# Optimization experiments

Hardware: AMD Instinct MI355X
Metric: run time of the kernel (lower is better)

The kernel has to match this reference:

```python
import jax, jax.numpy as jnp
import numpy as np

D_MODEL = 512
N_HEADS = 8
HEAD_DIM = D_MODEL // N_HEADS


def setup_inputs() -> dict:
    key = jax.random.key(0)
    ks = jax.random.split(key, 7)
    x = jax.random.normal(ks[0], (8, 2048, D_MODEL), dtype=jnp.float32)
    ln_gamma = jnp.ones((D_MODEL,), jnp.float32)
    ln_beta = jnp.zeros((D_MODEL,), jnp.float32)
    s = 1.0 / np.sqrt(D_MODEL)
    W_qkv = jax.random.uniform(ks[1], (3 * D_MODEL, D_MODEL), jnp.float32, -s, s)
    b_qkv = jax.random.uniform(ks[2], (3 * D_MODEL,), jnp.float32, -s, s)
    W_out = jax.random.uniform(ks[3], (D_MODEL, D_MODEL), jnp.float32, -s, s)
    b_out = jax.random.uniform(ks[4], (D_MODEL,), jnp.float32, -s, s)
    return {"x": x, "ln_gamma": ln_gamma, "ln_beta": ln_beta,
            "W_qkv": W_qkv, "b_qkv": b_qkv, "W_out": W_out, "b_out": b_out}


def reference(x, ln_gamma, ln_beta, W_qkv, b_qkv, W_out, b_out):
    b, s, d = x.shape
    # LayerNorm (eps=1e-5, torch default)
    mu = jnp.mean(x, axis=-1, keepdims=True)
    var = jnp.mean(jnp.square(x - mu), axis=-1, keepdims=True)
    xn = (x - mu) * jax.lax.rsqrt(var + 1e-5) * ln_gamma + ln_beta
    # QKV projection (torch Linear: x @ W.T + b)
    qkv = xn @ W_qkv.T + b_qkv                       # [b, s, 3d]
    qkv = qkv.reshape(b, s, 3, N_HEADS, HEAD_DIM)
    qkv = jnp.transpose(qkv, (2, 0, 3, 1, 4))        # [3, b, h, s, hd]
    q, k, v = qkv[0], qkv[1], qkv[2]
    scale = HEAD_DIM ** -0.5
    attn = jnp.einsum('bhqd,bhkd->bhqk', q, k) * scale
    attn = jax.nn.softmax(attn, axis=-1)
    out = jnp.einsum('bhqk,bhkd->bhqd', attn, v)     # [b, h, s, hd]
    out = jnp.transpose(out, (0, 2, 1, 3)).reshape(b, s, d)
    return out @ W_out.T + b_out
```

## Files before the change

kernel.cpp:

```cpp
#include <hip/hip_runtime.h>
#include <stdint.h>

#define NH 8
#define HD 64
#define BATCH 8
#define SEQ 2048
#define DM 512
#define TOK (BATCH * SEQ)

#define QSCALE 0.18033688011112042f

typedef __attribute__((ext_vector_type(8))) __bf16 bf16x8;
typedef __attribute__((ext_vector_type(4))) float f32x4;
typedef __attribute__((ext_vector_type(16))) float f32x16;
typedef __attribute__((ext_vector_type(8))) uint16_t u16x8;

__device__ __forceinline__ uint16_t f2bf(float f) {
  union { __bf16 h; uint16_t u; } c;
  c.h = (__bf16)f;
  return c.u;
}

__device__ __forceinline__ void load_lds16(const void* g, void* l) {
  __builtin_amdgcn_global_load_lds(
      (const __attribute__((address_space(1))) void*)g,
      (__attribute__((address_space(3))) void*)l, 16, 0, 0);
}

#define VM_DRAIN() asm volatile("s_waitcnt vmcnt(0)" ::: "memory")

__device__ __forceinline__ int swz128(int row, int kbyte) {
  return (row * 128 + kbyte) ^ ((row & 7) << 4);
}

#define MFMA16(a, b, c) __builtin_amdgcn_mfma_f32_16x16x32_bf16(a, b, c, 0, 0, 0)
#define MFMA32(a, b, c) __builtin_amdgcn_mfma_f32_32x32x16_bf16(a, b, c, 0, 0, 0)

__global__ __launch_bounds__(256) void ln_kernel(
    const float* __restrict__ x, const float* __restrict__ gam,
    const float* __restrict__ bet, uint16_t* __restrict__ xn) {
  const int row = blockIdx.x * 4 + (threadIdx.x >> 6);
  const int lane = threadIdx.x & 63;
  const float4* xr = (const float4*)(x + (size_t)row * DM);
  float4 a0 = xr[lane * 2 + 0];
  float4 a1 = xr[lane * 2 + 1];
  float s = a0.x + a0.y + a0.z + a0.w + a1.x + a1.y + a1.z + a1.w;
  float q = a0.x * a0.x + a0.y * a0.y + a0.z * a0.z + a0.w * a0.w +
            a1.x * a1.x + a1.y * a1.y + a1.z * a1.z + a1.w * a1.w;
#pragma unroll
  for (int m = 1; m < 64; m <<= 1) {
    s += __shfl_xor(s, m);
    q += __shfl_xor(q, m);
  }
  const float mean = s * (1.0f / DM);
  const float var = q * (1.0f / DM) - mean * mean;
  const float rstd = rsqrtf(var + 1e-5f);
  const float4* gv = (const float4*)gam;
  const float4* bv = (const float4*)bet;
  float4 g0 = gv[lane * 2], g1 = gv[lane * 2 + 1];
  float4 b0 = bv[lane * 2], b1 = bv[lane * 2 + 1];
  u16x8 r;
  r[0] = f2bf((a0.x - mean) * rstd * g0.x + b0.x);
  r[1] = f2bf((a0.y - mean) * rstd * g0.y + b0.y);
  r[2] = f2bf((a0.z - mean) * rstd * g0.z + b0.z);
  r[3] = f2bf((a0.w - mean) * rstd * g0.w + b0.w);
  r[4] = f2bf((a1.x - mean) * rstd * g1.x + b1.x);
  r[5] = f2bf((a1.y - mean) * rstd * g1.y + b1.y);
  r[6] = f2bf((a1.z - mean) * rstd * g1.z + b1.z);
  r[7] = f2bf((a1.w - mean) * rstd * g1.w + b1.w);
  *(u16x8*)(xn + (size_t)row * DM + lane * 8) = r;
}

__global__ __launch_bounds__(256) void cast_w(const float* __restrict__ w,
                                              uint16_t* __restrict__ o, int n8) {
  int i = blockIdx.x * 256 + threadIdx.x;
  if (i >= n8) return;
  const float4* p = (const float4*)w + (size_t)i * 2;
  float4 a0 = p[0], a1 = p[1];
  u16x8 r;
  r[0] = f2bf(a0.x); r[1] = f2bf(a0.y); r[2] = f2bf(a0.z); r[3] = f2bf(a0.w);
  r[4] = f2bf(a1.x); r[5] = f2bf(a1.y); r[6] = f2bf(a1.z); r[7] = f2bf(a1.w);
  *(u16x8*)(o + (size_t)i * 8) = r;
}

template <int EPI>
__global__ __launch_bounds__(256) void gemm_nt(
    const uint16_t* __restrict__ A, const uint16_t* __restrict__ Bw,
    const float* __restrict__ bias, uint16_t* __restrict__ oq,
    uint16_t* __restrict__ okk, uint16_t* __restrict__ ov,
    float* __restrict__ oc) {
  __shared__ __align__(16) char As[128 * 64 * 2];
  __shared__ __align__(16) char Bs[128 * 64 * 2];
  const int tid = threadIdx.x;
  const int lane = tid & 63;
  const int w = tid >> 6;
  const int wr = (w >> 1) * 64;
  const int wc = (w & 1) * 64;
  const int l15 = lane & 15;
  const int l4 = lane >> 4;
  const size_t tileM = (size_t)blockIdx.y * 128;
  const int tileN = blockIdx.x * 128;
  const int trow = tid >> 3;
  const int tcol = tid & 7;
  const f32x4 vzero = {0.f, 0.f, 0.f, 0.f};

  f32x4 acc[4][4];
#pragma unroll
  for (int m = 0; m < 4; ++m)
#pragma unroll
    for (int n = 0; n < 4; ++n) acc[m][n] = vzero;

  for (int kt = 0; kt < 8; ++kt) {
    if (kt) __syncthreads();
#pragma unroll
    for (int i = 0; i < 4; ++i) {
      const int row = i * 32 + trow;
      const int c0 = 8 * (tcol ^ (row & 7));
      load_lds16(A + (tileM + row) * DM + kt * 64 + c0, As + i * 4096 + w * 1024);
      load_lds16(Bw + (size_t)(tileN + row) * DM + kt * 64 + c0, Bs + i * 4096 + w * 1024);
    }
    VM_DRAIN();
    __syncthreads();
#pragma unroll
    for (int ks = 0; ks < 2; ++ks) {
      const int kb = ks * 64 + l4 * 16;
      bf16x8 af[4], bfr[4];
#pragma unroll
      for (int m = 0; m < 4; ++m) {
        const int r = wr + m * 16 + l15;
        af[m] = *(const bf16x8*)(As + swz128(r, kb));
      }
#pragma unroll
      for (int n = 0; n < 4; ++n) {
        const int r = wc + n * 16 + l15;
        bfr[n] = *(const bf16x8*)(Bs + swz128(r, kb));
      }
#pragma unroll
      for (int m = 0; m < 4; ++m)
#pragma unroll
        for (int n = 0; n < 4; ++n)
          acc[m][n] = MFMA16(af[m], bfr[n], acc[m][n]);
    }
  }

#pragma unroll
  for (int m = 0; m < 4; ++m) {
    const size_t row0 = tileM + wr + m * 16 + l4 * 4;
#pragma unroll
    for (int n = 0; n < 4; ++n) {
      const int col = tileN + wc + n * 16 + l15;
      const float bb = bias[col];
#pragma unroll
      for (int jj = 0; jj < 4; ++jj) {
        const float val = acc[m][n][jj] + bb;
        const size_t r = row0 + jj;
        if (EPI == 0) {
          const int wh = col >> 9;
          const int rem = col & 511;
          const int h = rem >> 6;
          const int dd = rem & 63;
          const int bi = (int)(r >> 11);
          const int si = (int)(r & 2047);
          const size_t bh = (size_t)bi * NH + h;
          if (wh == 0)
            oq[(bh * SEQ + si) * HD + dd] = f2bf(val * QSCALE);
          else if (wh == 1)
            okk[(bh * SEQ + si) * HD + dd] = f2bf(val);
          else
            ov[(bh * HD + dd) * SEQ + si] = f2bf(val);
        } else {
          oc[r * DM + col] = val;
        }
      }
    }
  }
}

__global__ __launch_bounds__(256) void attn_kernel(
    const uint16_t* __restrict__ qb, const uint16_t* __restrict__ kb,
    const uint16_t* __restrict__ vb, uint16_t* __restrict__ ab) {
  __shared__ __align__(16) char Ks[64 * 128];
  __shared__ __align__(16) char Vs[64 * 128];
  __shared__ float corrbuf[4 * 32];
  const int tid = threadIdx.x;
  const int lane = tid & 63;
  const int wq = tid >> 6;
  const int l31 = lane & 31;
  const int h = lane >> 5;
  const int bh = blockIdx.x >> 4;
  const int qt = blockIdx.x & 15;
  const uint16_t* qp = qb + (size_t)bh * SEQ * HD;
  const uint16_t* kp = kb + (size_t)bh * SEQ * HD;
  const uint16_t* vp = vb + (size_t)bh * HD * SEQ;
  const int trow = tid >> 3;
  const int tcol = tid & 7;

  auto stageK = [&](int tt) {
    const int kv0 = tt * 64;
#pragma unroll
    for (int i = 0; i < 2; ++i) {
      const int row = i * 32 + trow;
      const int c0 = 8 * (tcol ^ (row & 7));
      load_lds16(kp + (size_t)(kv0 + row) * HD + c0, Ks + i * 4096 + wq * 1024);
    }
  };
  auto stageV = [&](int tt) {
    const int kv0 = tt * 64;
#pragma unroll
    for (int i = 0; i < 2; ++i) {
      const int row = i * 32 + trow;
      const int c0 = 8 * (tcol ^ (row & 7));
      load_lds16(vp + (size_t)row * SEQ + kv0 + c0, Vs + i * 4096 + wq * 1024);
    }
  };

  bf16x8 qf[4];
  const int q0 = qt * 128 + wq * 32;
#pragma unroll
  for (int c = 0; c < 4; ++c)
    qf[c] = *(const bf16x8*)(qp + (size_t)(q0 + l31) * HD + c * 16 + h * 8);

  bf16x8 vone;
#pragma unroll
  for (int i = 0; i < 8; ++i) vone[i] = (__bf16)1.0f;

  f32x16 oacc0, oacc1, osum;
#pragma unroll
  for (int r = 0; r < 16; ++r) { oacc0[r] = 0.f; oacc1[r] = 0.f; osum[r] = 0.f; }
  float mrow = -1e30f;

  auto build2 = [&](const f32x16& s, float m, bf16x8* fa, bf16x8* fb) {
    uint32_t u[8];
#pragma unroll
    for (int i2 = 0; i2 < 8; ++i2) {
      float plo = exp2f(s[2 * i2] - m);
      float phi = exp2f(s[2 * i2 + 1] - m);
      asm("v_cvt_pk_bf16_f32 %0, %1, %2" : "=v"(u[i2]) : "v"(plo), "v"(phi));
    }
    asm("v_permlane32_swap_b32 %0, %1" : "+v"(u[0]), "+v"(u[2]));
    asm("v_permlane32_swap_b32 %0, %1" : "+v"(u[1]), "+v"(u[3]));
    asm("v_permlane32_swap_b32 %0, %1" : "+v"(u[4]), "+v"(u[6]));
    asm("v_permlane32_swap_b32 %0, %1" : "+v"(u[5]), "+v"(u[7]));
    union { uint32_t w[4]; bf16x8 v; } A, B;
    A.w[0] = u[0]; A.w[1] = u[1]; A.w[2] = u[2]; A.w[3] = u[3];
    B.w[0] = u[4]; B.w[1] = u[5]; B.w[2] = u[6]; B.w[3] = u[7];
    *fa = A.v; *fb = B.v;
  };

  stageK(0);
  stageV(0);

  for (int t = 0; t < SEQ / 64; ++t) {
    VM_DRAIN();
    __syncthreads();
    if (t) stageV(t);

    f32x16 s0, s1;
#pragma unroll
    for (int r = 0; r < 16; ++r) { s0[r] = 0.f; s1[r] = 0.f; }
#pragma unroll
    for (int c = 0; c < 4; ++c) {
      const int kbyte = c * 32 + h * 16;
      bf16x8 kf0 = *(const bf16x8*)(Ks + swz128(l31, kbyte));
      bf16x8 kf1 = *(const bf16x8*)(Ks + swz128(32 + l31, kbyte));
      s0 = MFMA32(kf0, qf[c], s0);
      s1 = MFMA32(kf1, qf[c], s1);
    }

    float r8[8];
#pragma unroll
    for (int i = 0; i < 8; ++i)
      r8[i] = fmaxf(fmaxf(s0[2 * i], s0[2 * i + 1]), fmaxf(s1[2 * i], s1[2 * i + 1]));
    float mx = fmaxf(fmaxf(fmaxf(r8[0], r8[1]), fmaxf(r8[2], r8[3])),
                     fmaxf(fmaxf(r8[4], r8[5]), fmaxf(r8[6], r8[7])));
    mx = fmaxf(mx, __shfl_xor(mx, 32));
    const float mold = mrow;
    const float mnew = fmaxf(mold, mx);
    const float corr = exp2f(mold - mnew);
    mrow = mnew;

    corrbuf[wq * 32 + l31] = corr;
    float4 cg[4];
#pragma unroll
    for (int g = 0; g < 4; ++g)
      cg[g] = *(const float4*)(corrbuf + wq * 32 + 8 * g + 4 * h);
#pragma unroll
    for (int rg = 0; rg < 4; ++rg)
#pragma unroll
      for (int rj = 0; rj < 4; ++rj) {
        const float cc = cg[rg][rj];
        const int r = rg * 4 + rj;
        oacc0[r] *= cc; oacc1[r] *= cc; osum[r] *= cc;
      }

    bf16x8 pa[4];
    build2(s0, mrow, &pa[0], &pa[1]);
    build2(s1, mrow, &pa[2], &pa[3]);

    VM_DRAIN();
    __syncthreads();
    if (t + 1 < SEQ / 64) stageK(t + 1);

#pragma unroll
    for (int i = 0; i < 4; ++i) {
      const int kbyte = i * 32 + h * 16;
      bf16x8 v0 = *(const bf16x8*)(Vs + swz128(l31, kbyte));
      bf16x8 v1 = *(const bf16x8*)(Vs + swz128(32 + l31, kbyte));
      oacc0 = MFMA32(pa[i], v0, oacc0);
      oacc1 = MFMA32(pa[i], v1, oacc1);
      osum = MFMA32(pa[i], vone, osum);
    }
  }

  const int bi = bh >> 3;
  const int head = bh & 7;
#pragma unroll
  for (int r = 0; r < 16; ++r) {
    const float inv = 1.0f / osum[r];
    const int q = (r & 3) + 8 * (r >> 2) + 4 * h;
    const size_t tok = (size_t)bi * SEQ + qt * 128 + wq * 32 + q;
    ab[tok * DM + head * HD + l31] = f2bf(oacc0[r] * inv);
    ab[tok * DM + head * HD + 32 + l31] = f2bf(oacc1[r] * inv);
  }
}

extern "C" void kernel_launch(void* const* d_in, const int* in_sizes, int n_in,
                              void* d_out, int out_size, void* d_ws, size_t ws_size,
                              hipStream_t stream) {
  const float* x = (const float*)d_in[0];
  const float* gam = (const float*)d_in[1];
  const float* bet = (const float*)d_in[2];
  const float* wqkv = (const float*)d_in[3];
  const float* bqkv = (const float*)d_in[4];
  const float* wout = (const float*)d_in[5];
  const float* bout = (const float*)d_in[6];

  const size_t SZ_XN = (size_t)TOK * DM * 2;
  const size_t SZ_WQ = (size_t)3 * DM * DM * 2;
  const size_t SZ_WO = (size_t)DM * DM * 2;
  const size_t SZ_HDBUF = (size_t)BATCH * NH * SEQ * HD * 2;

  char* p = (char*)d_ws;
  uint16_t* xn = (uint16_t*)p;      p += SZ_XN;
  uint16_t* wq = (uint16_t*)p;      p += SZ_WQ;
  uint16_t* wo = (uint16_t*)p;      p += SZ_WO;
  uint16_t* qbuf = (uint16_t*)p;    p += SZ_HDBUF;
  uint16_t* kbuf = (uint16_t*)p;    p += SZ_HDBUF;
  uint16_t* vbuf = (uint16_t*)p;    p += SZ_HDBUF;
  uint16_t* abuf = xn;

  ln_kernel<<<dim3(TOK / 4), dim3(256), 0, stream>>>(x, gam, bet, xn);
  cast_w<<<dim3((3 * DM * DM / 8) / 256), dim3(256), 0, stream>>>(wqkv, wq, 3 * DM * DM / 8);
  cast_w<<<dim3((DM * DM / 8) / 256), dim3(256), 0, stream>>>(wout, wo, DM * DM / 8);
  gemm_nt<0><<<dim3(12, 128), dim3(256), 0, stream>>>(xn, wq, bqkv, qbuf, kbuf, vbuf, nullptr);
  attn_kernel<<<dim3(BATCH * NH * (SEQ / 128)), dim3(256), 0, stream>>>(qbuf, kbuf, vbuf, abuf);
  gemm_nt<1><<<dim3(4, 128), dim3(256), 0, stream>>>(abuf, wo, bout, nullptr, nullptr, nullptr,
                                                     (float*)d_out);
}
```

Baseline: 229.6 us.

## Skip softmax rescale when max unchanged, use max3, setprio around MFMAs, hoist staging addresses

New measurement: 231.6 us. About the same (+0.9%).

```diff
diff --git a/kernel.cpp b/kernel.cpp
--- a/kernel.cpp
+++ b/kernel.cpp
@@ -28,6 +28,12 @@
 }
 
 #define VM_DRAIN() asm volatile("s_waitcnt vmcnt(0)" ::: "memory")
+
+__device__ __forceinline__ float fmax3(float a, float b, float c) {
+  float d;
+  asm("v_max3_f32 %0, %1, %2, %3" : "=v"(d) : "v"(a), "v"(b), "v"(c));
+  return d;
+}
 
 __device__ __forceinline__ int swz128(int row, int kbyte) {
   return (row * 128 + kbyte) ^ ((row & 7) << 4);
@@ -195,23 +201,19 @@
   const int trow = tid >> 3;
   const int tcol = tid & 7;
 
+  const int c0 = 8 * (tcol ^ (trow & 7));
+  const uint16_t* kSt = kp + (size_t)trow * HD + c0;
+  const uint16_t* vSt = vp + (size_t)trow * SEQ + c0;
+  char* ldsK = Ks + wq * 1024;
+  char* ldsV = Vs + wq * 1024;
+
   auto stageK = [&](int tt) {
-    const int kv0 = tt * 64;
-#pragma unroll
-    for (int i = 0; i < 2; ++i) {
-      const int row = i * 32 + trow;
-      const int c0 = 8 * (tcol ^ (row & 7));
-      load_lds16(kp + (size_t)(kv0 + row) * HD + c0, Ks + i * 4096 + wq * 1024);
-    }
+    load_lds16(kSt + tt * 4096, ldsK);
+    load_lds16(kSt + tt * 4096 + 2048, ldsK + 4096);
   };
   auto stageV = [&](int tt) {
-    const int kv0 = tt * 64;
-#pragma unroll
-    for (int i = 0; i < 2; ++i) {
-      const int row = i * 32 + trow;
-      const int c0 = 8 * (tcol ^ (row & 7));
-      load_lds16(vp + (size_t)row * SEQ + kv0 + c0, Vs + i * 4096 + wq * 1024);
-    }
+    load_lds16(vSt + tt * 64, ldsV);
+    load_lds16(vSt + tt * 64 + 32 * SEQ, ldsV + 4096);
   };
 
   bf16x8 qf[4];
@@ -258,6 +260,7 @@
     f32x16 s0, s1;
 #pragma unroll
     for (int r = 0; r < 16; ++r) { s0[r] = 0.f; s1[r] = 0.f; }
+    __builtin_amdgcn_s_setprio(1);
 #pragma unroll
     for (int c = 0; c < 4; ++c) {
       const int kbyte = c * 32 + h * 16;
@@ -266,32 +269,44 @@
       s0 = MFMA32(kf0, qf[c], s0);
       s1 = MFMA32(kf1, qf[c], s1);
     }
-
-    float r8[8];
-#pragma unroll
-    for (int i = 0; i < 8; ++i)
-      r8[i] = fmaxf(fmaxf(s0[2 * i], s0[2 * i + 1]), fmaxf(s1[2 * i], s1[2 * i + 1]));
-    float mx = fmaxf(fmaxf(fmaxf(r8[0], r8[1]), fmaxf(r8[2], r8[3])),
-                     fmaxf(fmaxf(r8[4], r8[5]), fmaxf(r8[6], r8[7])));
+    __builtin_amdgcn_s_setprio(0);
+
+    float a0 = fmax3(s0[0], s0[1], s0[2]);
+    float a1 = fmax3(s0[3], s0[4], s0[5]);
+    float a2 = fmax3(s0[6], s0[7], s0[8]);
+    float a3 = fmax3(s0[9], s0[10], s0[11]);
+    float a4 = fmax3(s0[12], s0[13], s0[14]);
+    float a5 = fmax3(s0[15], s1[0], s1[1]);
+    float a6 = fmax3(s1[2], s1[3], s1[4]);
+    float a7 = fmax3(s1[5], s1[6], s1[7]);
+    float a8 = fmax3(s1[8], s1[9], s1[10]);
+    float a9 = fmax3(s1[11], s1[12], s1[13]);
+    float a10 = fmaxf(s1[14], s1[15]);
+    float b0 = fmax3(a0, a1, a2);
+    float b1 = fmax3(a3, a4, a5);
+    float b2 = fmax3(a6, a7, a8);
+    float b3 = fmax3(a9, a10, b0);
+    float mx = fmax3(b1, b2, b3);
     mx = fmaxf(mx, __shfl_xor(mx, 32));
-    const float mold = mrow;
-    const float mnew = fmaxf(mold, mx);
-    const float corr = exp2f(mold - mnew);
-    mrow = mnew;
-
-    corrbuf[wq * 32 + l31] = corr;
-    float4 cg[4];
-#pragma unroll
-    for (int g = 0; g < 4; ++g)
-      cg[g] = *(const float4*)(corrbuf + wq * 32 + 8 * g + 4 * h);
-#pragma unroll
-    for (int rg = 0; rg < 4; ++rg)
-#pragma unroll
-      for (int rj = 0; rj < 4; ++rj) {
-        const float cc = cg[rg][rj];
-        const int r = rg * 4 + rj;
-        oacc0[r] *= cc; oacc1[r] *= cc; osum[r] *= cc;
-      }
+
+    if (__any(mx > mrow)) {
+      const float mnew = fmaxf(mrow, mx);
+      const float corr = exp2f(mrow - mnew);
+      mrow = mnew;
+      if (h == 0) corrbuf[wq * 32 + l31] = corr;
+      float4 cg[4];
+#pragma unroll
+      for (int g = 0; g < 4; ++g)
+        cg[g] = *(const float4*)(corrbuf + wq * 32 + 8 * g + 4 * h);
+#pragma unroll
+      for (int rg = 0; rg < 4; ++rg)
+#pragma unroll
+        for (int rj = 0; rj < 4; ++rj) {
+          const float cc = cg[rg][rj];
+          const int r = rg * 4 + rj;
+          oacc0[r] *= cc; oacc1[r] *= cc; osum[r] *= cc;
+        }
+    }
 
     bf16x8 pa[4];
     build2(s0, mrow, &pa[0], &pa[1]);
@@ -301,6 +316,7 @@
     __syncthreads();
     if (t + 1 < SEQ / 64) stageK(t + 1);
 
+    __builtin_amdgcn_s_setprio(1);
 #pragma unroll
     for (int i = 0; i < 4; ++i) {
       const int kbyte = i * 32 + h * 16;
@@ -310,6 +326,7 @@
       oacc1 = MFMA32(pa[i], v1, oacc1);
       osum = MFMA32(pa[i], vone, osum);
     }
+    __builtin_amdgcn_s_setprio(0);
   }
 
   const int bi = bh >> 3;
```

## Double-buffer K/V tiles in attention kernel with one barrier per iteration

Applied to the files above, without the earlier changes.

Measured after the change: 323.0 us. 40.7% more time.

```diff
diff --git a/kernel.cpp b/kernel.cpp
--- a/kernel.cpp
+++ b/kernel.cpp
@@ -179,8 +179,8 @@
 __global__ __launch_bounds__(256) void attn_kernel(
     const uint16_t* __restrict__ qb, const uint16_t* __restrict__ kb,
     const uint16_t* __restrict__ vb, uint16_t* __restrict__ ab) {
-  __shared__ __align__(16) char Ks[64 * 128];
-  __shared__ __align__(16) char Vs[64 * 128];
+  __shared__ __align__(16) char Ks[2 * 64 * 128];
+  __shared__ __align__(16) char Vs[2 * 64 * 128];
   __shared__ float corrbuf[4 * 32];
   const int tid = threadIdx.x;
   const int lane = tid & 63;
@@ -195,22 +195,24 @@
   const int trow = tid >> 3;
   const int tcol = tid & 7;
 
-  auto stageK = [&](int tt) {
+  auto stageK = [&](int tt, int buf) {
     const int kv0 = tt * 64;
 #pragma unroll
     for (int i = 0; i < 2; ++i) {
       const int row = i * 32 + trow;
       const int c0 = 8 * (tcol ^ (row & 7));
-      load_lds16(kp + (size_t)(kv0 + row) * HD + c0, Ks + i * 4096 + wq * 1024);
+      load_lds16(kp + (size_t)(kv0 + row) * HD + c0,
+                 Ks + buf * 8192 + i * 4096 + wq * 1024);
     }
   };
-  auto stageV = [&](int tt) {
+  auto stageV = [&](int tt, int buf) {
     const int kv0 = tt * 64;
 #pragma unroll
     for (int i = 0; i < 2; ++i) {
       const int row = i * 32 + trow;
       const int c0 = 8 * (tcol ^ (row & 7));
-      load_lds16(vp + (size_t)row * SEQ + kv0 + c0, Vs + i * 4096 + wq * 1024);
+      load_lds16(vp + (size_t)row * SEQ + kv0 + c0,
+                 Vs + buf * 8192 + i * 4096 + wq * 1024);
     }
   };
 
@@ -247,13 +249,19 @@
     *fa = A.v; *fb = B.v;
   };
 
-  stageK(0);
-  stageV(0);
-
+  stageK(0, 0);
+  stageV(0, 0);
+  VM_DRAIN();
+  __syncthreads();
+
+  int cur = 0;
   for (int t = 0; t < SEQ / 64; ++t) {
-    VM_DRAIN();
-    __syncthreads();
-    if (t) stageV(t);
+    if (t + 1 < SEQ / 64) {
+      stageK(t + 1, cur ^ 1);
+      stageV(t + 1, cur ^ 1);
+    }
+    const char* Kc = Ks + cur * 8192;
+    const char* Vc = Vs + cur * 8192;
 
     f32x16 s0, s1;
 #pragma unroll
@@ -261,8 +269,8 @@
 #pragma unroll
     for (int c = 0; c < 4; ++c) {
       const int kbyte = c * 32 + h * 16;
-      bf16x8 kf0 = *(const bf16x8*)(Ks + swz128(l31, kbyte));
-      bf16x8 kf1 = *(const bf16x8*)(Ks + swz128(32 + l31, kbyte));
+      bf16x8 kf0 = *(const bf16x8*)(Kc + swz128(l31, kbyte));
+      bf16x8 kf1 = *(const bf16x8*)(Kc + swz128(32 + l31, kbyte));
       s0 = MFMA32(kf0, qf[c], s0);
       s1 = MFMA32(kf1, qf[c], s1);
     }
@@ -297,19 +305,19 @@
     build2(s0, mrow, &pa[0], &pa[1]);
     build2(s1, mrow, &pa[2], &pa[3]);
 
-    VM_DRAIN();
-    __syncthreads();
-    if (t + 1 < SEQ / 64) stageK(t + 1);
-
 #pragma unroll
     for (int i = 0; i < 4; ++i) {
       const int kbyte = i * 32 + h * 16;
-      bf16x8 v0 = *(const bf16x8*)(Vs + swz128(l31, kbyte));
-      bf16x8 v1 = *(const bf16x8*)(Vs + swz128(32 + l31, kbyte));
+      bf16x8 v0 = *(const bf16x8*)(Vc + swz128(l31, kbyte));
+      bf16x8 v1 = *(const bf16x8*)(Vc + swz128(32 + l31, kbyte));
       oacc0 = MFMA32(pa[i], v0, oacc0);
       oacc1 = MFMA32(pa[i], v1, oacc1);
       osum = MFMA32(pa[i], vone, osum);
     }
+
+    VM_DRAIN();
+    __syncthreads();
+    cur ^= 1;
   }
 
   const int bi = bh >> 3;
```
